# Kernel optimization log

Hardware: AMD Instinct MI355X
Metric: run time of the kernel (lower is better)

Reference implementation:

```python
import jax, jax.numpy as jnp
import numpy as np

D = 768        # embed_dim
H = 12         # num_heads
DEPTH = 12
P = 16         # patch size
IMG = 224
G = IMG // P   # 14 patches per side
NPATCH = G * G # 196
N = NPATCH + 1 # seq len with cls token
MLP = 4 * D    # 3072
NC = 1000      # num_classes
EPS = 1e-6


def _ln(x, w, b):
    m = jnp.mean(x, axis=-1, keepdims=True)
    v = jnp.mean((x - m) ** 2, axis=-1, keepdims=True)
    return (x - m) / jnp.sqrt(v + EPS) * w + b


def setup_inputs() -> dict:
    key = jax.random.key(0)
    ks = jax.random.split(key, 12)
    f = lambda k, s: jax.random.normal(k, s, jnp.float32) * 0.02
    return {
        "x": jax.random.normal(ks[0], (32, 3, IMG, IMG), jnp.float32),
        "patch_w": f(ks[1], (3 * P * P, D)),  # Conv2d(3,768,16,16) as matmul
        "patch_b": jnp.zeros((D,), jnp.float32),
        "cls_token": f(ks[2], (1, 1, D)),
        "pos_embed": f(ks[3], (1, N, D)),
        "ln1_w": jnp.ones((DEPTH, D), jnp.float32),
        "ln1_b": jnp.zeros((DEPTH, D), jnp.float32),
        "qkv_w": f(ks[4], (DEPTH, D, 3 * D)),
        "qkv_b": jnp.zeros((DEPTH, 3 * D), jnp.float32),
        "proj_w": f(ks[5], (DEPTH, D, D)),
        "proj_b": jnp.zeros((DEPTH, D), jnp.float32),
        "ln2_w": jnp.ones((DEPTH, D), jnp.float32),
        "ln2_b": jnp.zeros((DEPTH, D), jnp.float32),
        "fc1_w": f(ks[6], (DEPTH, D, MLP)),
        "fc1_b": jnp.zeros((DEPTH, MLP), jnp.float32),
        "fc2_w": f(ks[7], (DEPTH, MLP, D)),
        "fc2_b": jnp.zeros((DEPTH, D), jnp.float32),
        "normf_w": jnp.ones((D,), jnp.float32),
        "normf_b": jnp.zeros((D,), jnp.float32),
        "head_w": f(ks[8], (D, NC)),
        "head_b": jnp.zeros((NC,), jnp.float32),
    }


def _fwd(x, patch_w, patch_b, cls_token, pos_embed, ln1_w, ln1_b, qkv_w, qkv_b,
         proj_w, proj_b, ln2_w, ln2_b, fc1_w, fc1_b, fc2_w, fc2_b,
         normf_w, normf_b, head_w, head_b):
    B = x.shape[0]
    # Patch embed: equivalent to Conv2d(3, D, kernel=16, stride=16)
    patches = x.reshape(B, 3, G, P, G, P).transpose(0, 2, 4, 1, 3, 5)
    patches = patches.reshape(B, NPATCH, 3 * P * P)
    h = patches @ patch_w + patch_b                       # [B, 196, D]
    cls = jnp.broadcast_to(cls_token, (B, 1, D))
    h = jnp.concatenate([cls, h], axis=1) + pos_embed     # [B, N, D]
    scale = (D // H) ** -0.5

    def block(h, p):
        l1w, l1b, qw, qb, pw, pb, l2w, l2b, f1w, f1b, f2w, f2b = p
        y = _ln(h, l1w, l1b)
        qkv = (y @ qw + qb).reshape(B, N, 3, H, D // H).transpose(2, 0, 3, 1, 4)
        q, k, v = qkv[0], qkv[1], qkv[2]                  # [B, H, N, dh]
        attn = jax.nn.softmax(jnp.einsum('bhnd,bhmd->bhnm', q, k) * scale, axis=-1)
        o = jnp.einsum('bhnm,bhmd->bhnd', attn, v).transpose(0, 2, 1, 3).reshape(B, N, D)
        h = h + (o @ pw + pb)
        y = _ln(h, l2w, l2b)
        h = h + (jax.nn.gelu(y @ f1w + f1b, approximate=False) @ f2w + f2b)
        return h, None

    params = (ln1_w, ln1_b, qkv_w, qkv_b, proj_w, proj_b,
              ln2_w, ln2_b, fc1_w, fc1_b, fc2_w, fc2_b)
    h, _ = jax.lax.scan(block, h, params)
    h = _ln(h, normf_w, normf_b)
    return h[:, 0] @ head_w + head_b                      # [B, 1000]


def reference(x, patch_w, patch_b, cls_token, pos_embed, ln1_w, ln1_b, qkv_w, qkv_b,
              proj_w, proj_b, ln2_w, ln2_b, fc1_w, fc1_b, fc2_w, fc2_b,
              normf_w, normf_b, head_w, head_b):
    return _fwd(x, patch_w, patch_b, cls_token, pos_embed, ln1_w, ln1_b, qkv_w, qkv_b,
                proj_w, proj_b, ln2_w, ln2_b, fc1_w, fc1_b, fc2_w, fc2_b,
                normf_w, normf_b, head_w, head_b)
```

## Files before the change

### kernel.cpp

```cpp
#include <hip/hip_runtime.h>
#include <hip/hip_bf16.h>
#include <type_traits>


#define BV   32
#define DIM  768
#define NHD  12
#define DH   64
#define NSEQ 197
#define NPAT 196
#define MLPD 3072
#define NCLS 1000
#define NLAYER 12

typedef __hip_bfloat16 bf16;
typedef __attribute__((ext_vector_type(8))) short s8v;
typedef __attribute__((ext_vector_type(4))) float f32x4;

#define GLDS16(gp, lp) __builtin_amdgcn_global_load_lds( \
    (const __attribute__((address_space(1))) void*)(gp), \
    (__attribute__((address_space(3))) void*)(lp), 16, 0, 0)

__device__ __forceinline__ short f2bf(float v) {
    return (short)__bfloat16_as_ushort(__float2bfloat16(v));
}

template<int ACT, bool RESID, typename TO>
__global__ __launch_bounds__(256)
void bgemm(const bf16* __restrict__ A, const bf16* __restrict__ B,
           const float* __restrict__ bias, TO* __restrict__ C,
           int M, int N, int K, int lda, int ldb, int ldc)
{
    __shared__ short As[24576];

    int nbx = gridDim.x;
    int nb  = nbx * gridDim.y;
    int bid = blockIdx.y * nbx + blockIdx.x;
    {
        int per = nb >> 3, rem = nb & 7;
        int x = bid & 7, loc = bid >> 3;
        bid = x * per + (x < rem ? x : rem) + loc;
    }
    const int m0 = (bid / nbx) * 128;
    const int n0 = (bid % nbx) * 128;

    const int tid  = threadIdx.x;
    const int wave = tid >> 6;
    const int lane = tid & 63;

    const int c0 = wave * 2, c1 = c0 + 1;
    const int rsub = lane >> 2;
    const int kp8  = (((lane & 3) ^ ((rsub >> 1) & 3)) * 8);

    int ra0 = m0 + c0 * 16 + rsub; if (ra0 > M - 1) ra0 = M - 1;
    int ra1 = m0 + c1 * 16 + rsub; if (ra1 > M - 1) ra1 = M - 1;
    int rb0 = n0 + c0 * 16 + rsub; if (rb0 > N - 1) rb0 = N - 1;
    int rb1 = n0 + c1 * 16 + rsub; if (rb1 > N - 1) rb1 = N - 1;

    const bf16* pa0 = A + (long)ra0 * lda + kp8;
    const bf16* pa1 = A + (long)ra1 * lda + kp8;
    const bf16* pb0 = B + (long)rb0 * ldb + kp8;
    const bf16* pb1 = B + (long)rb1 * ldb + kp8;

    const int wm = wave >> 1, wn = wave & 1;
    const int colr = lane & 15;
    const int quad = lane >> 4;

    f32x4 acc[4][4];
    #pragma unroll
    for (int i = 0; i < 4; ++i)
        #pragma unroll
        for (int j = 0; j < 4; ++j)
            acc[i][j] = (f32x4){0.f, 0.f, 0.f, 0.f};

    const int sq = quad ^ ((colr >> 1) & 3);
    const short* AsP = &As[(wm * 64 + colr) * 32 + sq * 8];
    const short* BsP = &As[4096 + (wn * 64 + colr) * 32 + sq * 8];

#define STAGE(bufi) do {                              \
        int _o = (bufi) * 8192;                       \
        GLDS16(pa0, &As[_o + c0 * 512]);              \
        GLDS16(pa1, &As[_o + c1 * 512]);              \
        GLDS16(pb0, &As[_o + 4096 + c0 * 512]);       \
        GLDS16(pb1, &As[_o + 4096 + c1 * 512]);       \
        pa0 += 32; pa1 += 32; pb0 += 32; pb1 += 32;   \
    } while (0)

    const int nt = K >> 5;
    STAGE(0);
    STAGE(1);
    int cur = 0, nxt = 2;

    for (int t = 0; t < nt; ++t) {
        if (t + 2 < nt) {
            STAGE(nxt);
            nxt = (nxt == 2) ? 0 : nxt + 1;
            asm volatile("s_waitcnt vmcnt(8)" ::: "memory");
        } else if (t + 1 < nt) {
            asm volatile("s_waitcnt vmcnt(4)" ::: "memory");
        } else {
            asm volatile("s_waitcnt vmcnt(0)" ::: "memory");
        }
        __builtin_amdgcn_s_barrier();
        asm volatile("" ::: "memory");

        const short* Ab = AsP + cur * 8192;
        const short* Bb = BsP + cur * 8192;
        s8v a[4], b[4];
        #pragma unroll
        for (int i = 0; i < 4; ++i) a[i] = *(const s8v*)(Ab + i * 512);
        #pragma unroll
        for (int j = 0; j < 4; ++j) b[j] = *(const s8v*)(Bb + j * 512);
        #pragma unroll
        for (int i = 0; i < 4; ++i)
            #pragma unroll
            for (int j = 0; j < 4; ++j)
                acc[i][j] = __builtin_amdgcn_mfma_f32_16x16x32_bf16(
                    a[i], b[j], acc[i][j], 0, 0, 0);

        cur = (cur == 2) ? 0 : cur + 1;
        asm volatile("" ::: "memory");
        __builtin_amdgcn_s_barrier();
        asm volatile("" ::: "memory");
    }
#undef STAGE

    float* ep = ((float*)As) + wave * 1024;
    const int lrow = lane >> 2;
    const int lc4  = (lane & 3) * 16;

    #pragma unroll
    for (int i = 0; i < 4; ++i) {
        #pragma unroll
        for (int j = 0; j < 4; ++j)
            #pragma unroll
            for (int r = 0; r < 4; ++r)
                ep[(quad * 4 + r) * 64 + j * 16 + colr] = acc[i][j][r];
        __syncthreads();

        int gm = m0 + wm * 64 + i * 16 + lrow;
        int gn = n0 + wn * 64 + lc4;
        if (gm < M) {
            float vals[16];
            #pragma unroll
            for (int c = 0; c < 16; ++c) vals[c] = ep[lrow * 64 + lc4 + c];

            if (gn + 16 <= N) {
                if (bias) {
                    #pragma unroll
                    for (int c = 0; c < 16; ++c) vals[c] += bias[gn + c];
                }
                if (ACT == 1) {
                    #pragma unroll
                    for (int c = 0; c < 16; ++c)
                        vals[c] = 0.5f * vals[c] *
                                  (1.0f + erff(vals[c] * 0.70710678118654752f));
                }
                if constexpr (std::is_same<TO, float>::value) {
                    float* Cp = (float*)C + (long)gm * ldc + gn;
                    if constexpr (RESID) {
                        #pragma unroll
                        for (int c4 = 0; c4 < 4; ++c4) {
                            f32x4 old = *(const f32x4*)&Cp[c4 * 4];
                            #pragma unroll
                            for (int e = 0; e < 4; ++e) vals[c4 * 4 + e] += old[e];
                        }
                    }
                    #pragma unroll
                    for (int c4 = 0; c4 < 4; ++c4) {
                        f32x4 v;
                        #pragma unroll
                        for (int e = 0; e < 4; ++e) v[e] = vals[c4 * 4 + e];
                        *(f32x4*)&Cp[c4 * 4] = v;
                    }
                } else {
                    short* Cp = (short*)C + (long)gm * ldc + gn;
                    s8v v0, v1;
                    #pragma unroll
                    for (int e = 0; e < 8; ++e) { v0[e] = f2bf(vals[e]); v1[e] = f2bf(vals[8 + e]); }
                    *(s8v*)&Cp[0] = v0;
                    *(s8v*)&Cp[8] = v1;
                }
            } else {
                #pragma unroll
                for (int c = 0; c < 16; ++c) {
                    int g = gn + c;
                    if (g >= N) continue;
                    float v = vals[c];
                    if (bias) v += bias[g];
                    if (ACT == 1) v = 0.5f * v * (1.0f + erff(v * 0.70710678118654752f));
                    long idx = (long)gm * ldc + g;
                    if constexpr (RESID) v += ((const float*)C)[idx];
                    if constexpr (std::is_same<TO, float>::value) C[idx] = v;
                    else C[idx] = __float2bfloat16(v);
                }
            }
        }
        __syncthreads();
    }
}

__global__ __launch_bounds__(256)
void attn_kernel(const bf16* __restrict__ qkv, bf16* __restrict__ O)
{
    __shared__ short Qs[64 * 72];
    __shared__ short Ks[224 * 72];
    __shared__ short Vt[64 * 224];

    const int tid  = threadIdx.x;
    const int wave = tid >> 6;
    const int lane = tid & 63;
    const int q0 = blockIdx.x * 64;
    const int b  = blockIdx.y / NHD;
    const int h  = blockIdx.y % NHD;
    const bf16* base = qkv + (long)b * NSEQ * (3 * DIM);

    #pragma unroll
    for (int p = 0; p < 2; ++p) {
        int idx = p * 2048 + tid * 8;
        int row = idx >> 6, col = idx & 63;
        int gr = q0 + row; if (gr > NSEQ - 1) gr = NSEQ - 1;
        *(s8v*)&Qs[row * 72 + col] =
            *(const s8v*)&base[(long)gr * (3 * DIM) + h * DH + col];
    }
    #pragma unroll
    for (int p = 0; p < 7; ++p) {
        int idx = p * 2048 + tid * 8;
        int row = idx >> 6, col = idx & 63;
        int gr = row; if (gr > NSEQ - 1) gr = NSEQ - 1;
        *(s8v*)&Ks[row * 72 + col] =
            *(const s8v*)&base[(long)gr * (3 * DIM) + DIM + h * DH + col];
    }
    {
        int seqL = tid & 31, dc = tid >> 5;
        #pragma unroll
        for (int st = 0; st < 7; ++st) {
            int seq = st * 32 + seqL;
            int gr = seq; if (gr > NSEQ - 1) gr = NSEQ - 1;
            s8v v = *(const s8v*)&base[(long)gr * (3 * DIM) + 2 * DIM + h * DH + dc * 8];
            #pragma unroll
            for (int i = 0; i < 8; ++i)
                Vt[(dc * 8 + i) * 224 + seq] = v[i];
        }
    }
    __syncthreads();

    const int colr = lane & 15;
    const int quad = lane >> 4;

    f32x4 s[14];
    #pragma unroll
    for (int j = 0; j < 14; ++j) s[j] = (f32x4){0.f, 0.f, 0.f, 0.f};
    #pragma unroll
    for (int kk = 0; kk < 2; ++kk) {
        s8v a = *(const s8v*)&Qs[(wave * 16 + colr) * 72 + quad * 8 + kk * 32];
        #pragma unroll
        for (int j = 0; j < 14; ++j) {
            s8v bf = *(const s8v*)&Ks[(j * 16 + colr) * 72 + quad * 8 + kk * 32];
            s[j] = __builtin_amdgcn_mfma_f32_16x16x32_bf16(a, bf, s[j], 0, 0, 0);
        }
    }

    float mx[4] = {-1e30f, -1e30f, -1e30f, -1e30f};
    #pragma unroll
    for (int j = 0; j < 14; ++j) {
        int c = j * 16 + colr;
        #pragma unroll
        for (int r = 0; r < 4; ++r) {
            s[j][r] *= 0.125f;
            if (c < NSEQ) mx[r] = fmaxf(mx[r], s[j][r]);
        }
    }
    #pragma unroll
    for (int off = 1; off <= 8; off <<= 1)
        #pragma unroll
        for (int r = 0; r < 4; ++r)
            mx[r] = fmaxf(mx[r], __shfl_xor(mx[r], off));

    float sum[4] = {0.f, 0.f, 0.f, 0.f};
    #pragma unroll
    for (int j = 0; j < 14; ++j) {
        int c = j * 16 + colr;
        #pragma unroll
        for (int r = 0; r < 4; ++r) {
            float v = (c < NSEQ) ? expf(s[j][r] - mx[r]) : 0.f;
            s[j][r] = v;
            sum[r] += v;
        }
    }
    #pragma unroll
    for (int off = 1; off <= 8; off <<= 1)
        #pragma unroll
        for (int r = 0; r < 4; ++r)
            sum[r] += __shfl_xor(sum[r], off);
    float inv[4];
    #pragma unroll
    for (int r = 0; r < 4; ++r) inv[r] = 1.0f / sum[r];

    __syncthreads();
    short* P = Ks;
    #pragma unroll
    for (int j = 0; j < 14; ++j)
        #pragma unroll
        for (int r = 0; r < 4; ++r)
            P[(wave * 16 + quad * 4 + r) * 224 + j * 16 + colr] =
                f2bf(s[j][r] * inv[r]);

    f32x4 o[4];
    #pragma unroll
    for (int j2 = 0; j2 < 4; ++j2) o[j2] = (f32x4){0.f, 0.f, 0.f, 0.f};
    #pragma unroll
    for (int ks = 0; ks < 7; ++ks) {
        s8v a = *(const s8v*)&P[(wave * 16 + colr) * 224 + quad * 8 + ks * 32];
        #pragma unroll
        for (int j2 = 0; j2 < 4; ++j2) {
            s8v bf = *(const s8v*)&Vt[(j2 * 16 + colr) * 224 + quad * 8 + ks * 32];
            o[j2] = __builtin_amdgcn_mfma_f32_16x16x32_bf16(a, bf, o[j2], 0, 0, 0);
        }
    }

    #pragma unroll
    for (int j2 = 0; j2 < 4; ++j2)
        #pragma unroll
        for (int r = 0; r < 4; ++r) {
            int qrow = q0 + wave * 16 + quad * 4 + r;
            if (qrow < NSEQ)
                O[((long)b * NSEQ + qrow) * DIM + h * DH + j2 * 16 + colr] =
                    __float2bfloat16(o[j2][r]);
        }
}

__global__ __launch_bounds__(256)
void wconv_kernel(const float* __restrict__ in, bf16* __restrict__ out,
                  int R, int C)
{
    __shared__ float t[32][33];
    int c0 = blockIdx.x * 32, r0 = blockIdx.y * 32;
    int tx = threadIdx.x & 31, ty = threadIdx.x >> 5;
    #pragma unroll
    for (int i = 0; i < 4; ++i) {
        int r = r0 + ty + 8 * i;
        if (r < R && c0 + tx < C) t[ty + 8 * i][tx] = in[(long)r * C + c0 + tx];
    }
    __syncthreads();
    #pragma unroll
    for (int i = 0; i < 4; ++i) {
        int c = c0 + ty + 8 * i;
        int r = r0 + tx;
        if (c < C && r < R) out[(long)c * R + r] = __float2bfloat16(t[tx][ty + 8 * i]);
    }
}

__global__ __launch_bounds__(256)
void ln_kernel(const float* __restrict__ in, long in_stride,
               bf16* __restrict__ out, long out_stride,
               const float* __restrict__ w, const float* __restrict__ b)
{
    long r = blockIdx.x;
    const float* x = in + r * in_stride;
    bf16* y = out + r * out_stride;
    int tid = threadIdx.x;

    float s = 0.f, s2 = 0.f;
    for (int i = tid; i < DIM; i += 256) {
        float v = x[i];
        s += v; s2 += v * v;
    }
    #pragma unroll
    for (int off = 32; off > 0; off >>= 1) {
        s  += __shfl_down(s, off);
        s2 += __shfl_down(s2, off);
    }
    __shared__ float red[2][4];
    int wave = tid >> 6, lane = tid & 63;
    if (lane == 0) { red[0][wave] = s; red[1][wave] = s2; }
    __syncthreads();
    if (tid == 0) {
        float t  = red[0][0] + red[0][1] + red[0][2] + red[0][3];
        float t2 = red[1][0] + red[1][1] + red[1][2] + red[1][3];
        float mean = t / (float)DIM;
        float var  = t2 / (float)DIM - mean * mean;
        red[0][0] = mean;
        red[1][0] = 1.0f / sqrtf(var + 1e-6f);
    }
    __syncthreads();
    float mean = red[0][0], rstd = red[1][0];
    for (int i = tid; i < DIM; i += 256)
        y[i] = __float2bfloat16((x[i] - mean) * rstd * w[i] + b[i]);
}

__global__ __launch_bounds__(256)
void im2col_kernel(const float* __restrict__ x, bf16* __restrict__ out)
{
    long i = (long)blockIdx.x * 256 + threadIdx.x;
    const long total = (long)BV * NPAT * DIM;
    if (i >= total) return;
    int col = (int)(i % DIM);
    long row = i / DIM;
    int c  = col >> 8;
    int py = (col >> 4) & 15;
    int px = col & 15;
    int b  = (int)(row / NPAT);
    int pp = (int)(row % NPAT);
    int gy = pp / 14, gx = pp % 14;
    out[i] = __float2bfloat16(
        x[(((long)(b * 3 + c) * 224 + gy * 16 + py) * 224) + gx * 16 + px]);
}

__global__ __launch_bounds__(256)
void assemble_kernel(const float* __restrict__ tmp, const float* __restrict__ cls,
                     const float* __restrict__ pos, float* __restrict__ h)
{
    long i = (long)blockIdx.x * 256 + threadIdx.x;
    const long total = (long)BV * NSEQ * DIM;
    if (i >= total) return;
    int d = (int)(i % DIM);
    long row = i / DIM;
    int n = (int)(row % NSEQ);
    long b = row / NSEQ;
    float v;
    if (n == 0) v = cls[d];
    else        v = tmp[(b * NPAT + (n - 1)) * DIM + d];
    h[i] = v + pos[(long)n * DIM + d];
}

extern "C" void kernel_launch(void* const* d_in, const int* in_sizes, int n_in,
                              void* d_out, int out_size, void* d_ws, size_t ws_size,
                              hipStream_t stream)
{
    const float* x        = (const float*)d_in[0];
    const float* patch_w  = (const float*)d_in[1];
    const float* patch_b  = (const float*)d_in[2];
    const float* cls_tok  = (const float*)d_in[3];
    const float* pos_emb  = (const float*)d_in[4];
    const float* ln1_w    = (const float*)d_in[5];
    const float* ln1_b    = (const float*)d_in[6];
    const float* qkv_w    = (const float*)d_in[7];
    const float* qkv_b    = (const float*)d_in[8];
    const float* proj_w   = (const float*)d_in[9];
    const float* proj_b   = (const float*)d_in[10];
    const float* ln2_w    = (const float*)d_in[11];
    const float* ln2_b    = (const float*)d_in[12];
    const float* fc1_w    = (const float*)d_in[13];
    const float* fc1_b    = (const float*)d_in[14];
    const float* fc2_w    = (const float*)d_in[15];
    const float* fc2_b    = (const float*)d_in[16];
    const float* normf_w  = (const float*)d_in[17];
    const float* normf_b  = (const float*)d_in[18];
    const float* head_w   = (const float*)d_in[19];
    const float* head_b   = (const float*)d_in[20];
    float* out = (float*)d_out;

    const long M = (long)BV * NSEQ;
    const long MP = (long)BV * NPAT;

    float* h      = (float*)d_ws;
    float* ptmp   = h + 4841472L;
    bf16*  qkv    = (bf16*)(ptmp + 4816896L);
    bf16*  lnout  = qkv + 14524416L;
    bf16*  big    = lnout + 4841472L;
    bf16*  wT     = big + 19365888L;
    bf16*  qkvT = wT;
    bf16*  projT = wT + 1769472L;
    bf16*  fc1T  = wT + 2359296L;
    bf16*  fc2T  = wT + 4718592L;

    dim3 blk(256);

    wconv_kernel<<<dim3(24, 24), blk, 0, stream>>>(patch_w, qkvT, DIM, DIM);
    im2col_kernel<<<dim3((unsigned)((MP * DIM + 255) / 256)), blk, 0, stream>>>(x, big);
    bgemm<0, false, float><<<dim3(6, 49), blk, 0, stream>>>(
        big, qkvT, patch_b, ptmp, (int)MP, DIM, DIM, DIM, DIM, DIM);
    assemble_kernel<<<dim3((unsigned)((M * DIM + 255) / 256)), blk, 0, stream>>>(
        ptmp, cls_tok, pos_emb, h);

    for (int l = 0; l < NLAYER; ++l) {
        wconv_kernel<<<dim3(72, 24), blk, 0, stream>>>(
            qkv_w + (long)l * DIM * 3 * DIM, qkvT, DIM, 3 * DIM);
        wconv_kernel<<<dim3(24, 24), blk, 0, stream>>>(
            proj_w + (long)l * DIM * DIM, projT, DIM, DIM);
        wconv_kernel<<<dim3(96, 24), blk, 0, stream>>>(
            fc1_w + (long)l * DIM * MLPD, fc1T, DIM, MLPD);
        wconv_kernel<<<dim3(24, 96), blk, 0, stream>>>(
            fc2_w + (long)l * MLPD * DIM, fc2T, MLPD, DIM);

        ln_kernel<<<dim3((unsigned)M), blk, 0, stream>>>(
            h, DIM, lnout, DIM, ln1_w + (long)l * DIM, ln1_b + (long)l * DIM);

        bgemm<0, false, bf16><<<dim3(18, 50), blk, 0, stream>>>(
            lnout, qkvT, qkv_b + (long)l * 3 * DIM, qkv,
            (int)M, 3 * DIM, DIM, DIM, DIM, 3 * DIM);

        attn_kernel<<<dim3(4, BV * NHD), blk, 0, stream>>>(qkv, lnout);

        bgemm<0, true, float><<<dim3(6, 50), blk, 0, stream>>>(
            lnout, projT, proj_b + (long)l * DIM, h,
            (int)M, DIM, DIM, DIM, DIM, DIM);

        ln_kernel<<<dim3((unsigned)M), blk, 0, stream>>>(
            h, DIM, lnout, DIM, ln2_w + (long)l * DIM, ln2_b + (long)l * DIM);

        bgemm<1, false, bf16><<<dim3(24, 50), blk, 0, stream>>>(
            lnout, fc1T, fc1_b + (long)l * MLPD, big,
            (int)M, MLPD, DIM, DIM, DIM, MLPD);

        bgemm<0, true, float><<<dim3(6, 50), blk, 0, stream>>>(
            big, fc2T, fc2_b + (long)l * DIM, h,
            (int)M, DIM, MLPD, MLPD, MLPD, DIM);
    }

    ln_kernel<<<dim3(BV), blk, 0, stream>>>(
        h, (long)NSEQ * DIM, lnout, DIM, normf_w, normf_b);

    wconv_kernel<<<dim3(32, 24), blk, 0, stream>>>(head_w, qkvT, DIM, NCLS);
    bgemm<0, false, float><<<dim3(8, 1), blk, 0, stream>>>(
        lnout, qkvT, head_b, out, BV, NCLS, DIM, DIM, DIM, NCLS);
}
```

Before: 3.241 ms.

## Add 64-row GEMM tiles, fuse weight conversions, wave-per-row layernorm, register Q in attention

Templates the GEMM on the M-tile count so the narrow 768-column GEMMs (patch, proj, fc2, head) use 64-row tiles, doubling the block count to fill the 256 CUs better. The four per-layer weight transpose/convert launches are merged into one kernel, and layernorm becomes one wavefront per row with vectorized loads and shuffle-only reduction. Attention loads Q fragments straight into registers instead of staging them through shared memory. The smaller tiles trade lower data reuse per block for more parallelism, and an extra barrier is added in attention.

```diff
diff --git a/kernel.cpp b/kernel.cpp
--- a/kernel.cpp
+++ b/kernel.cpp
@@ -25,13 +25,16 @@
     return (short)__bfloat16_as_ushort(__float2bfloat16(v));
 }
 
-template<int ACT, bool RESID, typename TO>
+template<int ACT, bool RESID, typename TO, int MI>
 __global__ __launch_bounds__(256)
 void bgemm(const bf16* __restrict__ A, const bf16* __restrict__ B,
            const float* __restrict__ bias, TO* __restrict__ C,
            int M, int N, int K, int lda, int ldb, int ldc)
 {
-    __shared__ short As[24576];
+    constexpr int BM    = MI * 32;
+    constexpr int ASIZE = MI * 1024;
+    constexpr int BUFS  = ASIZE + 4096;
+    __shared__ short As[3 * BUFS];
 
     int nbx = gridDim.x;
     int nb  = nbx * gridDim.y;
@@ -41,7 +44,7 @@
         int x = bid & 7, loc = bid >> 3;
         bid = x * per + (x < rem ? x : rem) + loc;
     }
-    const int m0 = (bid / nbx) * 128;
+    const int m0 = (bid / nbx) * BM;
     const int n0 = (bid % nbx) * 128;
 
     const int tid  = threadIdx.x;
@@ -52,8 +55,11 @@
     const int rsub = lane >> 2;
     const int kp8  = (((lane & 3) ^ ((rsub >> 1) & 3)) * 8);
 
-    int ra0 = m0 + c0 * 16 + rsub; if (ra0 > M - 1) ra0 = M - 1;
-    int ra1 = m0 + c1 * 16 + rsub; if (ra1 > M - 1) ra1 = M - 1;
+    int ra0, ra1;
+    if constexpr (MI == 4) { ra0 = m0 + c0 * 16 + rsub; ra1 = m0 + c1 * 16 + rsub; }
+    else                   { ra0 = m0 + wave * 16 + rsub; ra1 = ra0; }
+    if (ra0 > M - 1) ra0 = M - 1;
+    if (ra1 > M - 1) ra1 = M - 1;
     int rb0 = n0 + c0 * 16 + rsub; if (rb0 > N - 1) rb0 = N - 1;
     int rb1 = n0 + c1 * 16 + rsub; if (rb1 > N - 1) rb1 = N - 1;
 
@@ -66,25 +72,30 @@
     const int colr = lane & 15;
     const int quad = lane >> 4;
 
-    f32x4 acc[4][4];
-    #pragma unroll
-    for (int i = 0; i < 4; ++i)
+    f32x4 acc[MI][4];
+    #pragma unroll
+    for (int i = 0; i < MI; ++i)
         #pragma unroll
         for (int j = 0; j < 4; ++j)
             acc[i][j] = (f32x4){0.f, 0.f, 0.f, 0.f};
 
     const int sq = quad ^ ((colr >> 1) & 3);
-    const short* AsP = &As[(wm * 64 + colr) * 32 + sq * 8];
-    const short* BsP = &As[4096 + (wn * 64 + colr) * 32 + sq * 8];
-
-#define STAGE(bufi) do {                              \
-        int _o = (bufi) * 8192;                       \
-        GLDS16(pa0, &As[_o + c0 * 512]);              \
-        GLDS16(pa1, &As[_o + c1 * 512]);              \
-        GLDS16(pb0, &As[_o + 4096 + c0 * 512]);       \
-        GLDS16(pb1, &As[_o + 4096 + c1 * 512]);       \
-        pa0 += 32; pa1 += 32; pb0 += 32; pb1 += 32;   \
-    } while (0)
+    const short* AsP = &As[(wm * (MI * 16) + colr) * 32 + sq * 8];
+    const short* BsP = &As[ASIZE + (wn * 64 + colr) * 32 + sq * 8];
+
+    auto STAGE = [&](int bufi) {
+        int _o = bufi * BUFS;
+        if constexpr (MI == 4) {
+            GLDS16(pa0, &As[_o + c0 * 512]);
+            GLDS16(pa1, &As[_o + c1 * 512]);
+            pa1 += 32;
+        } else {
+            GLDS16(pa0, &As[_o + wave * 512]);
+        }
+        GLDS16(pb0, &As[_o + ASIZE + c0 * 512]);
+        GLDS16(pb1, &As[_o + ASIZE + c1 * 512]);
+        pa0 += 32; pb0 += 32; pb1 += 32;
+    };
 
     const int nt = K >> 5;
     STAGE(0);
@@ -95,24 +106,26 @@
         if (t + 2 < nt) {
             STAGE(nxt);
             nxt = (nxt == 2) ? 0 : nxt + 1;
-            asm volatile("s_waitcnt vmcnt(8)" ::: "memory");
+            if constexpr (MI == 4) asm volatile("s_waitcnt vmcnt(8)" ::: "memory");
+            else                   asm volatile("s_waitcnt vmcnt(6)" ::: "memory");
         } else if (t + 1 < nt) {
-            asm volatile("s_waitcnt vmcnt(4)" ::: "memory");
+            if constexpr (MI == 4) asm volatile("s_waitcnt vmcnt(4)" ::: "memory");
+            else                   asm volatile("s_waitcnt vmcnt(3)" ::: "memory");
         } else {
             asm volatile("s_waitcnt vmcnt(0)" ::: "memory");
         }
         __builtin_amdgcn_s_barrier();
         asm volatile("" ::: "memory");
 
-        const short* Ab = AsP + cur * 8192;
-        const short* Bb = BsP + cur * 8192;
-        s8v a[4], b[4];
-        #pragma unroll
-        for (int i = 0; i < 4; ++i) a[i] = *(const s8v*)(Ab + i * 512);
+        const short* Ab = AsP + cur * BUFS;
+        const short* Bb = BsP + cur * BUFS;
+        s8v a[MI], b[4];
+        #pragma unroll
+        for (int i = 0; i < MI; ++i) a[i] = *(const s8v*)(Ab + i * 512);
         #pragma unroll
         for (int j = 0; j < 4; ++j) b[j] = *(const s8v*)(Bb + j * 512);
         #pragma unroll
-        for (int i = 0; i < 4; ++i)
+        for (int i = 0; i < MI; ++i)
             #pragma unroll
             for (int j = 0; j < 4; ++j)
                 acc[i][j] = __builtin_amdgcn_mfma_f32_16x16x32_bf16(
@@ -123,14 +136,13 @@
         __builtin_amdgcn_s_barrier();
         asm volatile("" ::: "memory");
     }
-#undef STAGE
 
     float* ep = ((float*)As) + wave * 1024;
     const int lrow = lane >> 2;
     const int lc4  = (lane & 3) * 16;
 
     #pragma unroll
-    for (int i = 0; i < 4; ++i) {
+    for (int i = 0; i < MI; ++i) {
         #pragma unroll
         for (int j = 0; j < 4; ++j)
             #pragma unroll
@@ -138,7 +150,7 @@
                 ep[(quad * 4 + r) * 64 + j * 16 + colr] = acc[i][j][r];
         __syncthreads();
 
-        int gm = m0 + wm * 64 + i * 16 + lrow;
+        int gm = m0 + wm * (MI * 16) + i * 16 + lrow;
         int gn = n0 + wn * 64 + lc4;
         if (gm < M) {
             float vals[16];
@@ -203,7 +215,6 @@
 __global__ __launch_bounds__(256)
 void attn_kernel(const bf16* __restrict__ qkv, bf16* __restrict__ O)
 {
-    __shared__ short Qs[64 * 72];
     __shared__ short Ks[224 * 72];
     __shared__ short Vt[64 * 224];
 
@@ -215,14 +226,14 @@
     const int h  = blockIdx.y % NHD;
     const bf16* base = qkv + (long)b * NSEQ * (3 * DIM);
 
-    #pragma unroll
-    for (int p = 0; p < 2; ++p) {
-        int idx = p * 2048 + tid * 8;
-        int row = idx >> 6, col = idx & 63;
-        int gr = q0 + row; if (gr > NSEQ - 1) gr = NSEQ - 1;
-        *(s8v*)&Qs[row * 72 + col] =
-            *(const s8v*)&base[(long)gr * (3 * DIM) + h * DH + col];
-    }
+    const int colr = lane & 15;
+    const int quad = lane >> 4;
+
+    int qr = q0 + wave * 16 + colr; if (qr > NSEQ - 1) qr = NSEQ - 1;
+    const bf16* qp = &base[(long)qr * (3 * DIM) + h * DH + quad * 8];
+    s8v qa0 = *(const s8v*)qp;
+    s8v qa1 = *(const s8v*)(qp + 32);
+
     #pragma unroll
     for (int p = 0; p < 7; ++p) {
         int idx = p * 2048 + tid * 8;
@@ -245,20 +256,15 @@
     }
     __syncthreads();
 
-    const int colr = lane & 15;
-    const int quad = lane >> 4;
-
     f32x4 s[14];
     #pragma unroll
     for (int j = 0; j < 14; ++j) s[j] = (f32x4){0.f, 0.f, 0.f, 0.f};
     #pragma unroll
-    for (int kk = 0; kk < 2; ++kk) {
-        s8v a = *(const s8v*)&Qs[(wave * 16 + colr) * 72 + quad * 8 + kk * 32];
-        #pragma unroll
-        for (int j = 0; j < 14; ++j) {
-            s8v bf = *(const s8v*)&Ks[(j * 16 + colr) * 72 + quad * 8 + kk * 32];
-            s[j] = __builtin_amdgcn_mfma_f32_16x16x32_bf16(a, bf, s[j], 0, 0, 0);
-        }
+    for (int j = 0; j < 14; ++j) {
+        s8v bf0 = *(const s8v*)&Ks[(j * 16 + colr) * 72 + quad * 8];
+        s[j] = __builtin_amdgcn_mfma_f32_16x16x32_bf16(qa0, bf0, s[j], 0, 0, 0);
+        s8v bf1 = *(const s8v*)&Ks[(j * 16 + colr) * 72 + quad * 8 + 32];
+        s[j] = __builtin_amdgcn_mfma_f32_16x16x32_bf16(qa1, bf1, s[j], 0, 0, 0);
     }
 
     float mx[4] = {-1e30f, -1e30f, -1e30f, -1e30f};
@@ -305,6 +311,8 @@
         for (int r = 0; r < 4; ++r)
             P[(wave * 16 + quad * 4 + r) * 224 + j * 16 + colr] =
                 f2bf(s[j][r] * inv[r]);
+
+    __syncthreads();
 
     f32x4 o[4];
     #pragma unroll
@@ -330,12 +338,12 @@
         }
 }
 
-__global__ __launch_bounds__(256)
-void wconv_kernel(const float* __restrict__ in, bf16* __restrict__ out,
-                  int R, int C)
+__device__ __forceinline__ void wconv_tile(const float* __restrict__ in,
+                                           bf16* __restrict__ out,
+                                           int R, int C, int bx, int by)
 {
     __shared__ float t[32][33];
-    int c0 = blockIdx.x * 32, r0 = blockIdx.y * 32;
+    int c0 = bx * 32, r0 = by * 32;
     int tx = threadIdx.x & 31, ty = threadIdx.x >> 5;
     #pragma unroll
     for (int i = 0; i < 4; ++i) {
@@ -352,41 +360,63 @@
 }
 
 __global__ __launch_bounds__(256)
+void wconv_kernel(const float* __restrict__ in, bf16* __restrict__ out,
+                  int R, int C)
+{
+    wconv_tile(in, out, R, C, blockIdx.x, blockIdx.y);
+}
+
+__global__ __launch_bounds__(256)
+void wconv4_kernel(const float* __restrict__ qw, const float* __restrict__ pw,
+                   const float* __restrict__ f1w, const float* __restrict__ f2w,
+                   bf16* __restrict__ qT, bf16* __restrict__ pT,
+                   bf16* __restrict__ f1T, bf16* __restrict__ f2T)
+{
+    int bid = blockIdx.x;
+    if (bid < 1728)      { int t = bid;        wconv_tile(qw,  qT,  768,  2304, t % 72, t / 72); }
+    else if (bid < 2304) { int t = bid - 1728; wconv_tile(pw,  pT,  768,  768,  t % 24, t / 24); }
+    else if (bid < 4608) { int t = bid - 2304; wconv_tile(f1w, f1T, 768,  3072, t % 96, t / 96); }
+    else                 { int t = bid - 4608; wconv_tile(f2w, f2T, 3072, 768,  t % 24, t / 24); }
+}
+
+__global__ __launch_bounds__(256)
 void ln_kernel(const float* __restrict__ in, long in_stride,
                bf16* __restrict__ out, long out_stride,
-               const float* __restrict__ w, const float* __restrict__ b)
-{
-    long r = blockIdx.x;
+               const float* __restrict__ w, const float* __restrict__ b,
+               int nrows)
+{
+    int wave = threadIdx.x >> 6, lane = threadIdx.x & 63;
+    long r = (long)blockIdx.x * 4 + wave;
+    if (r >= nrows) return;
     const float* x = in + r * in_stride;
     bf16* y = out + r * out_stride;
-    int tid = threadIdx.x;
-
+
+    f32x4 c[3];
     float s = 0.f, s2 = 0.f;
-    for (int i = tid; i < DIM; i += 256) {
-        float v = x[i];
-        s += v; s2 += v * v;
-    }
-    #pragma unroll
-    for (int off = 32; off > 0; off >>= 1) {
-        s  += __shfl_down(s, off);
-        s2 += __shfl_down(s2, off);
-    }
-    __shared__ float red[2][4];
-    int wave = tid >> 6, lane = tid & 63;
-    if (lane == 0) { red[0][wave] = s; red[1][wave] = s2; }
-    __syncthreads();
-    if (tid == 0) {
-        float t  = red[0][0] + red[0][1] + red[0][2] + red[0][3];
-        float t2 = red[1][0] + red[1][1] + red[1][2] + red[1][3];
-        float mean = t / (float)DIM;
-        float var  = t2 / (float)DIM - mean * mean;
-        red[0][0] = mean;
-        red[1][0] = 1.0f / sqrtf(var + 1e-6f);
-    }
-    __syncthreads();
-    float mean = red[0][0], rstd = red[1][0];
-    for (int i = tid; i < DIM; i += 256)
-        y[i] = __float2bfloat16((x[i] - mean) * rstd * w[i] + b[i]);
+    #pragma unroll
+    for (int p = 0; p < 3; ++p) {
+        c[p] = *(const f32x4*)&x[p * 256 + lane * 4];
+        #pragma unroll
+        for (int e = 0; e < 4; ++e) { s += c[p][e]; s2 += c[p][e] * c[p][e]; }
+    }
+    #pragma unroll
+    for (int off = 1; off <= 32; off <<= 1) {
+        s  += __shfl_xor(s, off);
+        s2 += __shfl_xor(s2, off);
+    }
+    float mean = s * (1.0f / (float)DIM);
+    float var  = s2 * (1.0f / (float)DIM) - mean * mean;
+    float rstd = 1.0f / sqrtf(var + 1e-6f);
+
+    #pragma unroll
+    for (int p = 0; p < 3; ++p) {
+        f32x4 wv = *(const f32x4*)&w[p * 256 + lane * 4];
+        f32x4 bv = *(const f32x4*)&b[p * 256 + lane * 4];
+        #pragma unroll
+        for (int e = 0; e < 4; ++e)
+            y[p * 256 + lane * 4 + e] =
+                __float2bfloat16((c[p][e] - mean) * rstd * wv[e] + bv[e]);
+    }
 }
 
 __global__ __launch_bounds__(256)
@@ -469,50 +499,46 @@
 
     wconv_kernel<<<dim3(24, 24), blk, 0, stream>>>(patch_w, qkvT, DIM, DIM);
     im2col_kernel<<<dim3((unsigned)((MP * DIM + 255) / 256)), blk, 0, stream>>>(x, big);
-    bgemm<0, false, float><<<dim3(6, 49), blk, 0, stream>>>(
+    bgemm<0, false, float, 2><<<dim3(6, 98), blk, 0, stream>>>(
         big, qkvT, patch_b, ptmp, (int)MP, DIM, DIM, DIM, DIM, DIM);
     assemble_kernel<<<dim3((unsigned)((M * DIM + 255) / 256)), blk, 0, stream>>>(
         ptmp, cls_tok, pos_emb, h);
 
     for (int l = 0; l < NLAYER; ++l) {
-        wconv_kernel<<<dim3(72, 24), blk, 0, stream>>>(
-            qkv_w + (long)l * DIM * 3 * DIM, qkvT, DIM, 3 * DIM);
-        wconv_kernel<<<dim3(24, 24), blk, 0, stream>>>(
-            proj_w + (long)l * DIM * DIM, projT, DIM, DIM);
-        wconv_kernel<<<dim3(96, 24), blk, 0, stream>>>(
-            fc1_w + (long)l * DIM * MLPD, fc1T, DIM, MLPD);
-        wconv_kernel<<<dim3(24, 96), blk, 0, stream>>>(
-            fc2_w + (long)l * MLPD * DIM, fc2T, MLPD, DIM);
-
-        ln_kernel<<<dim3((unsigned)M), blk, 0, stream>>>(
-            h, DIM, lnout, DIM, ln1_w + (long)l * DIM, ln1_b + (long)l * DIM);
-
-        bgemm<0, false, bf16><<<dim3(18, 50), blk, 0, stream>>>(
+        wconv4_kernel<<<dim3(6912), blk, 0, stream>>>(
+            qkv_w + (long)l * DIM * 3 * DIM, proj_w + (long)l * DIM * DIM,
+            fc1_w + (long)l * DIM * MLPD,    fc2_w + (long)l * MLPD * DIM,
+            qkvT, projT, fc1T, fc2T);
+
+        ln_kernel<<<dim3((unsigned)((M + 3) / 4)), blk, 0, stream>>>(
+            h, DIM, lnout, DIM, ln1_w + (long)l * DIM, ln1_b + (long)l * DIM, (int)M);
+
+        bgemm<0, false, bf16, 4><<<dim3(18, 50), blk, 0, stream>>>(
             lnout, qkvT, qkv_b + (long)l * 3 * DIM, qkv,
             (int)M, 3 * DIM, DIM, DIM, DIM, 3 * DIM);
 
         attn_kernel<<<dim3(4, BV * NHD), blk, 0, stream>>>(qkv, lnout);
 
-        bgemm<0, true, float><<<dim3(6, 50), blk, 0, stream>>>(
+        bgemm<0, true, float, 2><<<dim3(6, 99), blk, 0, stream>>>(
             lnout, projT, proj_b + (long)l * DIM, h,
             (int)M, DIM, DIM, DIM, DIM, DIM);
 
-        ln_kernel<<<dim3((unsigned)M), blk, 0, stream>>>(
-            h, DIM, lnout, DIM, ln2_w + (long)l * DIM, ln2_b + (long)l * DIM);
-
-        bgemm<1, false, bf16><<<dim3(24, 50), blk, 0, stream>>>(
+        ln_kernel<<<dim3((unsigned)((M + 3) / 4)), blk, 0, stream>>>(
+            h, DIM, lnout, DIM, ln2_w + (long)l * DIM, ln2_b + (long)l * DIM, (int)M);
+
+        bgemm<1, false, bf16, 4><<<dim3(24, 50), blk, 0, stream>>>(
             lnout, fc1T, fc1_b + (long)l * MLPD, big,
             (int)M, MLPD, DIM, DIM, DIM, MLPD);
 
-        bgemm<0, true, float><<<dim3(6, 50), blk, 0, stream>>>(
+        bgemm<0, true, float, 2><<<dim3(6, 99), blk, 0, stream>>>(
             big, fc2T, fc2_b + (long)l * DIM, h,
             (int)M, DIM, MLPD, MLPD, MLPD, DIM);
     }
 
-    ln_kernel<<<dim3(BV), blk, 0, stream>>>(
-        h, (long)NSEQ * DIM, lnout, DIM, normf_w, normf_b);
+    ln_kernel<<<dim3(8), blk, 0, stream>>>(
+        h, (long)NSEQ * DIM, lnout, DIM, normf_w, normf_b, BV);
 
     wconv_kernel<<<dim3(32, 24), blk, 0, stream>>>(head_w, qkvT, DIM, NCLS);
-    bgemm<0, false, float><<<dim3(8, 1), blk, 0, stream>>>(
+    bgemm<0, false, float, 2><<<dim3(8, 1), blk, 0, stream>>>(
         lnout, qkvT, head_b, out, BV, NCLS, DIM, DIM, DIM, NCLS);
 }
```

After: 3.112 ms. 1.04x faster.
